# Kernel tuning notes

Measured on AMD Instinct MI355X. Metric: run time of the kernel, lower is better.

## Reference

```python
import jax, jax.numpy as jnp
import numpy as np

EMB = 1024
HEADS = 16
HEAD_DIM = EMB // HEADS

def setup_inputs() -> dict:
    key = jax.random.key(0)
    ks = jax.random.split(key, 12)
    s = 0.02
    x = jax.random.normal(ks[0], (2, 2048, EMB), dtype=jnp.float32)
    return {
        "x": x,
        "wq": jax.random.normal(ks[1], (EMB, EMB), jnp.float32) * s,
        "bq": jnp.zeros((EMB,), jnp.float32),
        "wk": jax.random.normal(ks[2], (EMB, EMB), jnp.float32) * s,
        "bk": jnp.zeros((EMB,), jnp.float32),
        "wv": jax.random.normal(ks[3], (EMB, EMB), jnp.float32) * s,
        "bv": jnp.zeros((EMB,), jnp.float32),
        "wo": jax.random.normal(ks[4], (EMB, EMB), jnp.float32) * s,
        "bo": jnp.zeros((EMB,), jnp.float32),
        "gamma": jnp.ones((EMB,), jnp.float32),
        "beta": jnp.zeros((EMB,), jnp.float32),
    }

def _layernorm(x, gamma, beta, eps=1e-5):
    mu = jnp.mean(x, axis=-1, keepdims=True)
    var = jnp.mean(jnp.square(x - mu), axis=-1, keepdims=True)
    return (x - mu) * jax.lax.rsqrt(var + eps) * gamma + beta

def reference(x, wq, bq, wk, bk, wv, bv, wo, bo, gamma, beta):
    B, T, D = x.shape
    H, d_k = HEADS, HEAD_DIM
    # Linear(y = x W^T + b), then split heads
    q = (x @ wq.T + bq).reshape(B, T, H, d_k)
    k = (x @ wk.T + bk).reshape(B, T, H, d_k)
    v = (x @ wv.T + bv).reshape(B, T, H, d_k)
    scores = jnp.einsum('bthd,bshd->bhts', q, k) / jnp.sqrt(jnp.float32(d_k))
    attn = jax.nn.softmax(scores, axis=-1)  # dropout is identity in eval mode
    out = jnp.einsum('bhts,bshd->bthd', attn, v).reshape(B, T, D)
    out = out @ wo.T + bo
    return _layernorm(x + out, gamma, beta)
```

## Files before the change

kernel.cpp:

```cpp
#include <hip/hip_runtime.h>
#include <stdint.h>
#include <stddef.h>


typedef __bf16 bf16_t;
typedef bf16_t bf16x8 __attribute__((ext_vector_type(8)));
typedef float f32x16 __attribute__((ext_vector_type(16)));
typedef uint16_t u16x8 __attribute__((ext_vector_type(8)));

#define MFMA32(a, b, c) __builtin_amdgcn_mfma_f32_32x32x16_bf16((a), (b), (c), 0, 0, 0)

__device__ __forceinline__ uint16_t f2bf(float f) {
  __bf16 h = (__bf16)f;
  return *(uint16_t*)&h;
}

__device__ __forceinline__ void gload16(const void* g, void* l) {
  __builtin_amdgcn_global_load_lds((const __attribute__((address_space(1))) void*)g,
                                   (__attribute__((address_space(3))) void*)l,
                                   16, 0, 0);
}

__global__ __launch_bounds__(256) void cvt_all(
    const float* __restrict__ x, const float* __restrict__ wq,
    const float* __restrict__ wk, const float* __restrict__ wv,
    const float* __restrict__ wo, uint16_t* __restrict__ xb,
    uint16_t* __restrict__ wqb, uint16_t* __restrict__ wkb,
    uint16_t* __restrict__ wvb, uint16_t* __restrict__ wob) {
  const int gid = blockIdx.x * 256 + threadIdx.x;
  const float* src; uint16_t* dst; int off;
  if (gid < 1048576) {
    src = x; dst = xb; off = gid;
  } else {
    const int t = gid - 1048576;
    off = t & 262143;
    switch (t >> 18) {
      case 0: src = wq; dst = wqb; break;
      case 1: src = wk; dst = wkb; break;
      case 2: src = wv; dst = wvb; break;
      default: src = wo; dst = wob; break;
    }
  }
  const float4 f = ((const float4*)src)[off];
  uint64_t p = (uint64_t)f2bf(f.x) | ((uint64_t)f2bf(f.y) << 16) |
               ((uint64_t)f2bf(f.z) << 32) | ((uint64_t)f2bf(f.w) << 48);
  ((uint64_t*)dst)[off] = p;
}

template <bool OUT_BF16>
__device__ __forceinline__ void gemm128(const uint16_t* __restrict__ A,
                                        const uint16_t* __restrict__ Bt,
                                        const float* __restrict__ bias,
                                        float oscale,
                                        uint16_t* __restrict__ outb,
                                        float* __restrict__ outf) {
  __shared__ uint16_t sA[2][128 * 32];
  __shared__ uint16_t sB[2][128 * 32];
  const int tid = threadIdx.x;
  const int lane = tid & 63, w = tid >> 6;
  const int l31 = lane & 31, half = lane >> 5;
  const int m0 = blockIdx.y * 128, n0 = blockIdx.x * 128;
  const int wm = (w >> 1) * 64, wn = (w & 1) * 64;

  const int ch0 = tid, ch1 = tid + 256;
  const int r0 = ch0 >> 2, g0 = (((ch0 & 3) ^ (r0 & 3)) << 3);
  const int r1 = ch1 >> 2, g1 = (((ch1 & 3) ^ (r1 & 3)) << 3);
  const uint16_t* a0 = A + (size_t)(m0 + r0) * 1024 + g0;
  const uint16_t* a1 = A + (size_t)(m0 + r1) * 1024 + g1;
  const uint16_t* b0 = Bt + (size_t)(n0 + r0) * 1024 + g0;
  const uint16_t* b1 = Bt + (size_t)(n0 + r1) * 1024 + g1;

  gload16(a0, &sA[0][ch0 * 8]);
  gload16(a1, &sA[0][ch1 * 8]);
  gload16(b0, &sB[0][ch0 * 8]);
  gload16(b1, &sB[0][ch1 * 8]);

  f32x16 acc[2][2] = {};

  for (int kt = 0; kt < 32; ++kt) {
    __syncthreads();
    const int cur = kt & 1;
    if (kt < 31) {
      const int ko = (kt + 1) * 32;
      const int nxt = cur ^ 1;
      gload16(a0 + ko, &sA[nxt][ch0 * 8]);
      gload16(a1 + ko, &sA[nxt][ch1 * 8]);
      gload16(b0 + ko, &sB[nxt][ch0 * 8]);
      gload16(b1 + ko, &sB[nxt][ch1 * 8]);
    }
#pragma unroll
    for (int s = 0; s < 2; ++s) {
      const int c = s * 2 + half;
      bf16x8 af[2], bfr[2];
#pragma unroll
      for (int i = 0; i < 2; ++i) {
        const int arow = wm + i * 32 + l31;
        af[i] = *(const bf16x8*)&sA[cur][arow * 32 + ((c ^ (arow & 3)) << 3)];
      }
#pragma unroll
      for (int j = 0; j < 2; ++j) {
        const int brow = wn + j * 32 + l31;
        bfr[j] = *(const bf16x8*)&sB[cur][brow * 32 + ((c ^ (brow & 3)) << 3)];
      }
#pragma unroll
      for (int i = 0; i < 2; ++i)
#pragma unroll
        for (int j = 0; j < 2; ++j) acc[i][j] = MFMA32(af[i], bfr[j], acc[i][j]);
    }
  }

#pragma unroll
  for (int i = 0; i < 2; ++i) {
#pragma unroll
    for (int j = 0; j < 2; ++j) {
      const int gn = n0 + wn + j * 32 + l31;
      const float bv = bias[gn];
#pragma unroll
      for (int reg = 0; reg < 16; ++reg) {
        const int gm = m0 + wm + i * 32 + (reg & 3) + 8 * (reg >> 2) + 4 * half;
        const float v = (acc[i][j][reg] + bv) * oscale;
        const size_t idx = (size_t)gm * 1024 + gn;
        if constexpr (OUT_BF16) outb[idx] = f2bf(v);
        else outf[idx] = v;
      }
    }
  }
}

#define QSCALE 0.18033688011112042f

__global__ __launch_bounds__(256) void qkv_gemm(
    const uint16_t* __restrict__ xb, const uint16_t* __restrict__ wqb,
    const uint16_t* __restrict__ wkb, const uint16_t* __restrict__ wvb,
    const float* __restrict__ bq, const float* __restrict__ bk,
    const float* __restrict__ bv, uint16_t* __restrict__ qb,
    uint16_t* __restrict__ kb, uint16_t* __restrict__ vb) {
  const uint16_t* Bt; const float* bias; uint16_t* out; float sc;
  if (blockIdx.z == 0)      { Bt = wqb; bias = bq; out = qb; sc = QSCALE; }
  else if (blockIdx.z == 1) { Bt = wkb; bias = bk; out = kb; sc = 1.f; }
  else                      { Bt = wvb; bias = bv; out = vb; sc = 1.f; }
  gemm128<true>(xb, Bt, bias, sc, out, nullptr);
}

__global__ __launch_bounds__(256) void o_gemm(const uint16_t* __restrict__ ab,
                                              const uint16_t* __restrict__ wob,
                                              const float* __restrict__ bo,
                                              float* __restrict__ y) {
  gemm128<false>(ab, wob, bo, 1.f, nullptr, y);
}

__global__ __launch_bounds__(256) void v_trans(const uint16_t* __restrict__ vb,
                                               uint16_t* __restrict__ vbT) {
  __shared__ uint16_t sT[64 * 136];
  const int tid = threadIdx.x;
  const int t0 = blockIdx.x * 128;
  const int h = blockIdx.y, b = blockIdx.z;
#pragma unroll
  for (int c = 0; c < 4; ++c) {
    const int idx = c * 256 + tid;
    const int t = idx >> 3, d8 = (idx & 7) * 8;
    u16x8 v = *(const u16x8*)&vb[(size_t)(b * 2048 + t0 + t) * 1024 + h * 64 + d8];
#pragma unroll
    for (int e = 0; e < 8; ++e) sT[(d8 + e) * 136 + t] = v[e];
  }
  __syncthreads();
  const size_t obase = ((size_t)(b * 16 + h) * 64) * 2048 + t0;
#pragma unroll
  for (int c = 0; c < 4; ++c) {
    const int idx = c * 256 + tid;
    const int d = idx >> 4, t8 = (idx & 15) * 8;
    u16x8 v = *(const u16x8*)&sT[d * 136 + t8];
    *(u16x8*)&vbT[obase + (size_t)d * 2048 + t8] = v;
  }
}

__global__ __launch_bounds__(256) void attn(const uint16_t* __restrict__ qb,
                                            const uint16_t* __restrict__ kb,
                                            const uint16_t* __restrict__ vbT,
                                            uint16_t* __restrict__ ab) {
  __shared__ uint16_t sK[2][64 * 64];
  __shared__ uint16_t sV[2][64 * 64];
  __shared__ uint16_t sP[4][32 * 64];
  const int tid = threadIdx.x;
  const int lane = tid & 63, w = tid >> 6;
  const int l31 = lane & 31, half = lane >> 5;
  const int hb = blockIdx.x;
  const int h = hb & 15, b = hb >> 4;
  const int q0 = blockIdx.y * 128;
  const size_t qkbase = (size_t)b * 2048 * 1024 + (size_t)h * 64;
  const size_t vtbase = (size_t)hb * 64 * 2048;

  const int ch0 = tid, ch1 = tid + 256;
  const int r0 = ch0 >> 3, g0 = (((ch0 & 7) ^ (r0 & 7)) << 3);
  const int r1 = ch1 >> 3, g1 = (((ch1 & 7) ^ (r1 & 7)) << 3);
  const uint16_t* k0 = kb + qkbase + (size_t)r0 * 1024 + g0;
  const uint16_t* k1 = kb + qkbase + (size_t)r1 * 1024 + g1;
  const uint16_t* v0 = vbT + vtbase + (size_t)r0 * 2048 + g0;
  const uint16_t* v1 = vbT + vtbase + (size_t)r1 * 2048 + g1;

  gload16(k0, &sK[0][ch0 * 8]);
  gload16(k1, &sK[0][ch1 * 8]);
  gload16(v0, &sV[0][ch0 * 8]);
  gload16(v1, &sV[0][ch1 * 8]);

  bf16x8 qa[4];
  {
    const uint16_t* qrow =
        qb + qkbase + (size_t)(q0 + w * 32 + l31) * 1024 + half * 8;
#pragma unroll
    for (int s = 0; s < 4; ++s) qa[s] = *(const bf16x8*)(qrow + s * 16);
  }

  f32x16 acc_o[2] = {};
  float li[16];
#pragma unroll
  for (int r = 0; r < 16; ++r) li[r] = 0.f;

  uint16_t* sPw = sP[w];
  __bf16* sPb = (__bf16*)sPw;

  for (int kt = 0; kt < 32; ++kt) {
    __syncthreads();
    const int cur = kt & 1;
    if (kt < 31) {
      const size_t so = (size_t)(kt + 1) * 64;
      const int nxt = cur ^ 1;
      gload16(k0 + so * 1024, &sK[nxt][ch0 * 8]);
      gload16(k1 + so * 1024, &sK[nxt][ch1 * 8]);
      gload16(v0 + so, &sV[nxt][ch0 * 8]);
      gload16(v1 + so, &sV[nxt][ch1 * 8]);
    }

    f32x16 acc_s[2] = {};
#pragma unroll
    for (int s = 0; s < 4; ++s) {
      const int c = s * 2 + half;
#pragma unroll
      for (int n = 0; n < 2; ++n) {
        const int brow = n * 32 + l31;
        const bf16x8 kk =
            *(const bf16x8*)&sK[cur][brow * 64 + ((c ^ (brow & 7)) << 3)];
        acc_s[n] = MFMA32(qa[s], kk, acc_s[n]);
      }
    }

#pragma unroll
    for (int reg = 0; reg < 16; ++reg) {
      const int row = (reg & 3) + 8 * (reg >> 2) + 4 * half;
#pragma unroll
      for (int n = 0; n < 2; ++n) {
        const float p = __builtin_amdgcn_exp2f(acc_s[n][reg]);
        li[reg] += p;
        const int col = n * 32 + l31;
        sPb[row * 64 + (((col >> 3) ^ (row & 7)) << 3) + (col & 7)] = (__bf16)p;
      }
    }

#pragma unroll
    for (int s = 0; s < 4; ++s) {
      const int c = s * 2 + half;
      const bf16x8 pa =
          *(const bf16x8*)&sPw[l31 * 64 + ((c ^ (l31 & 7)) << 3)];
#pragma unroll
      for (int n = 0; n < 2; ++n) {
        const int vrow = n * 32 + l31;
        const bf16x8 vv =
            *(const bf16x8*)&sV[cur][vrow * 64 + ((c ^ (vrow & 7)) << 3)];
        acc_o[n] = MFMA32(pa, vv, acc_o[n]);
      }
    }
  }

#pragma unroll
  for (int reg = 0; reg < 16; ++reg) {
    float s = li[reg];
#pragma unroll
    for (int o = 1; o < 32; o <<= 1) s += __shfl_xor(s, o);
    li[reg] = 1.f / s;
  }

#pragma unroll
  for (int n = 0; n < 2; ++n)
#pragma unroll
    for (int reg = 0; reg < 16; ++reg) {
      const int row = q0 + w * 32 + (reg & 3) + 8 * (reg >> 2) + 4 * half;
      const int col = h * 64 + n * 32 + l31;
      ab[(size_t)(b * 2048 + row) * 1024 + col] = f2bf(acc_o[n][reg] * li[reg]);
    }
}

__global__ __launch_bounds__(256) void resid_ln(const float* __restrict__ x,
                                                const float* __restrict__ y,
                                                const float* __restrict__ gamma,
                                                const float* __restrict__ beta,
                                                float* __restrict__ out) {
  const int row = blockIdx.x, tid = threadIdx.x;
  const size_t base = (size_t)row * 1024 + tid * 4;
  const float4 xv = *(const float4*)(x + base);
  const float4 yv = *(const float4*)(y + base);
  const float a = xv.x + yv.x, b2 = xv.y + yv.y, c = xv.z + yv.z, d = xv.w + yv.w;
  float s = a + b2 + c + d;
#pragma unroll
  for (int o = 1; o < 64; o <<= 1) s += __shfl_xor(s, o);
  __shared__ float red[4];
  const int w = tid >> 6;
  if ((tid & 63) == 0) red[w] = s;
  __syncthreads();
  const float mu = (red[0] + red[1] + red[2] + red[3]) * (1.f / 1024.f);
  const float da = a - mu, db = b2 - mu, dc = c - mu, dd = d - mu;
  float sq = da * da + db * db + dc * dc + dd * dd;
#pragma unroll
  for (int o = 1; o < 64; o <<= 1) sq += __shfl_xor(sq, o);
  __syncthreads();
  if ((tid & 63) == 0) red[w] = sq;
  __syncthreads();
  const float var = (red[0] + red[1] + red[2] + red[3]) * (1.f / 1024.f);
  const float rs = rsqrtf(var + 1e-5f);
  const float4 g = *(const float4*)(gamma + tid * 4);
  const float4 bt = *(const float4*)(beta + tid * 4);
  float4 o4;
  o4.x = da * rs * g.x + bt.x;
  o4.y = db * rs * g.y + bt.y;
  o4.z = dc * rs * g.z + bt.z;
  o4.w = dd * rs * g.w + bt.w;
  *(float4*)(out + base) = o4;
}

extern "C" void kernel_launch(void* const* d_in, const int* in_sizes, int n_in,
                              void* d_out, int out_size, void* d_ws, size_t ws_size,
                              hipStream_t stream) {
  const float* x     = (const float*)d_in[0];
  const float* wq    = (const float*)d_in[1];
  const float* bq    = (const float*)d_in[2];
  const float* wk    = (const float*)d_in[3];
  const float* bk    = (const float*)d_in[4];
  const float* wv    = (const float*)d_in[5];
  const float* bv    = (const float*)d_in[6];
  const float* wo    = (const float*)d_in[7];
  const float* bo    = (const float*)d_in[8];
  const float* gamma = (const float*)d_in[9];
  const float* beta  = (const float*)d_in[10];
  float* out = (float*)d_out;
  char* ws = (char*)d_ws;
  const size_t MB = 1024 * 1024;
  uint16_t* xb  = (uint16_t*)(ws);
  uint16_t* ab  = xb;
  uint16_t* wqb = (uint16_t*)(ws + 8 * MB);
  uint16_t* wkb = (uint16_t*)(ws + 10 * MB);
  uint16_t* wvb = (uint16_t*)(ws + 12 * MB);
  uint16_t* wob = (uint16_t*)(ws + 14 * MB);
  uint16_t* qb  = (uint16_t*)(ws + 16 * MB);
  uint16_t* kb  = (uint16_t*)(ws + 24 * MB);
  uint16_t* vb  = (uint16_t*)(ws + 32 * MB);
  uint16_t* vbT = (uint16_t*)(ws + 40 * MB);
  float*    y   = (float*)(ws + 16 * MB);

  cvt_all<<<8192, 256, 0, stream>>>(x, wq, wk, wv, wo, xb, wqb, wkb, wvb, wob);
  qkv_gemm<<<dim3(8, 32, 3), 256, 0, stream>>>(xb, wqb, wkb, wvb, bq, bk, bv, qb, kb, vb);
  v_trans<<<dim3(16, 16, 2), 256, 0, stream>>>(vb, vbT);
  attn<<<dim3(32, 16), 256, 0, stream>>>(qb, kb, vbT, ab);
  o_gemm<<<dim3(8, 32), 256, 0, stream>>>(ab, wob, bo, y);
  resid_ln<<<4096, 256, 0, stream>>>(x, y, gamma, beta, out);
}
```

Baseline: 226.2 us.

## Split attention KV tiles across two wave groups with 512-thread blocks

The attention kernel now runs 8 waves per block. Two groups of four waves each take half of a 128-key tile, so each block loads 128 keys per iteration and runs 16 iterations instead of 32. The P tile is processed in 32-column halves per wave to cut LDS use, and partial outputs and row sums are merged through shared memory at the end. This adds parallel waves per block and halves the barrier count, at the cost of a cross-group reduction and more LDS per block, which may limit occupancy.

```diff
diff --git a/kernel.cpp b/kernel.cpp
--- a/kernel.cpp
+++ b/kernel.cpp
@@ -174,41 +174,45 @@
   }
 }
 
-__global__ __launch_bounds__(256) void attn(const uint16_t* __restrict__ qb,
-                                            const uint16_t* __restrict__ kb,
-                                            const uint16_t* __restrict__ vbT,
-                                            uint16_t* __restrict__ ab) {
-  __shared__ uint16_t sK[2][64 * 64];
-  __shared__ uint16_t sV[2][64 * 64];
-  __shared__ uint16_t sP[4][32 * 64];
+__global__ __launch_bounds__(512, 4) void attn(const uint16_t* __restrict__ qb,
+                                               const uint16_t* __restrict__ kb,
+                                               const uint16_t* __restrict__ vbT,
+                                               uint16_t* __restrict__ ab) {
+  __shared__ __align__(16) uint16_t smem[40960];
+  uint16_t* sK = smem;
+  uint16_t* sV = smem + 16384;
+  uint16_t* sP = smem + 32768;
   const int tid = threadIdx.x;
   const int lane = tid & 63, w = tid >> 6;
   const int l31 = lane & 31, half = lane >> 5;
+  const int rg = w & 3, sh = w >> 2;
   const int hb = blockIdx.x;
   const int h = hb & 15, b = hb >> 4;
   const int q0 = blockIdx.y * 128;
   const size_t qkbase = (size_t)b * 2048 * 1024 + (size_t)h * 64;
   const size_t vtbase = (size_t)hb * 64 * 2048;
 
-  const int ch0 = tid, ch1 = tid + 256;
-  const int r0 = ch0 >> 3, g0 = (((ch0 & 7) ^ (r0 & 7)) << 3);
-  const int r1 = ch1 >> 3, g1 = (((ch1 & 7) ^ (r1 & 7)) << 3);
-  const uint16_t* k0 = kb + qkbase + (size_t)r0 * 1024 + g0;
-  const uint16_t* k1 = kb + qkbase + (size_t)r1 * 1024 + g1;
-  const uint16_t* v0 = vbT + vtbase + (size_t)r0 * 2048 + g0;
-  const uint16_t* v1 = vbT + vtbase + (size_t)r1 * 2048 + g1;
-
-  gload16(k0, &sK[0][ch0 * 8]);
-  gload16(k1, &sK[0][ch1 * 8]);
-  gload16(v0, &sV[0][ch0 * 8]);
-  gload16(v1, &sV[0][ch1 * 8]);
+  const int ch0 = tid, ch1 = tid + 512;
+  const int kr0 = ch0 >> 3, kg0 = (((ch0 & 7) ^ (kr0 & 7)) << 3);
+  const int kr1 = ch1 >> 3, kg1 = (((ch1 & 7) ^ (kr1 & 7)) << 3);
+  const int vr0 = ch0 >> 4, vg0 = (((ch0 & 15) ^ (vr0 & 15)) << 3);
+  const int vr1 = ch1 >> 4, vg1 = (((ch1 & 15) ^ (vr1 & 15)) << 3);
+  const uint16_t* k0 = kb + qkbase + (size_t)kr0 * 1024 + kg0;
+  const uint16_t* k1 = kb + qkbase + (size_t)kr1 * 1024 + kg1;
+  const uint16_t* v0 = vbT + vtbase + (size_t)vr0 * 2048 + vg0;
+  const uint16_t* v1 = vbT + vtbase + (size_t)vr1 * 2048 + vg1;
+
+  gload16(k0, sK + ch0 * 8);
+  gload16(k1, sK + ch1 * 8);
+  gload16(v0, sV + ch0 * 8);
+  gload16(v1, sV + ch1 * 8);
 
   bf16x8 qa[4];
   {
     const uint16_t* qrow =
-        qb + qkbase + (size_t)(q0 + w * 32 + l31) * 1024 + half * 8;
-#pragma unroll
-    for (int s = 0; s < 4; ++s) qa[s] = *(const bf16x8*)(qrow + s * 16);
+        qb + qkbase + (size_t)(q0 + rg * 32 + l31) * 1024 + half * 8;
+#pragma unroll
+    for (int s4 = 0; s4 < 4; ++s4) qa[s4] = *(const bf16x8*)(qrow + s4 * 16);
   }
 
   f32x16 acc_o[2] = {};
@@ -216,77 +220,99 @@
 #pragma unroll
   for (int r = 0; r < 16; ++r) li[r] = 0.f;
 
-  uint16_t* sPw = sP[w];
+  uint16_t* sPw = sP + w * 1024;
   __bf16* sPb = (__bf16*)sPw;
 
-  for (int kt = 0; kt < 32; ++kt) {
+  for (int kt = 0; kt < 16; ++kt) {
     __syncthreads();
     const int cur = kt & 1;
-    if (kt < 31) {
-      const size_t so = (size_t)(kt + 1) * 64;
+    if (kt < 15) {
+      const size_t soK = (size_t)(kt + 1) * 128 * 1024;
+      const int soV = (kt + 1) * 128;
       const int nxt = cur ^ 1;
-      gload16(k0 + so * 1024, &sK[nxt][ch0 * 8]);
-      gload16(k1 + so * 1024, &sK[nxt][ch1 * 8]);
-      gload16(v0 + so, &sV[nxt][ch0 * 8]);
-      gload16(v1 + so, &sV[nxt][ch1 * 8]);
-    }
+      gload16(k0 + soK, sK + nxt * 8192 + ch0 * 8);
+      gload16(k1 + soK, sK + nxt * 8192 + ch1 * 8);
+      gload16(v0 + soV, sV + nxt * 8192 + ch0 * 8);
+      gload16(v1 + soV, sV + nxt * 8192 + ch1 * 8);
+    }
+    const uint16_t* sKc = sK + cur * 8192;
+    const uint16_t* sVc = sV + cur * 8192;
 
     f32x16 acc_s[2] = {};
 #pragma unroll
-    for (int s = 0; s < 4; ++s) {
-      const int c = s * 2 + half;
+    for (int s4 = 0; s4 < 4; ++s4) {
+      const int c = s4 * 2 + half;
 #pragma unroll
       for (int n = 0; n < 2; ++n) {
-        const int brow = n * 32 + l31;
+        const int brow = sh * 64 + n * 32 + l31;
         const bf16x8 kk =
-            *(const bf16x8*)&sK[cur][brow * 64 + ((c ^ (brow & 7)) << 3)];
-        acc_s[n] = MFMA32(qa[s], kk, acc_s[n]);
-      }
-    }
-
-#pragma unroll
-    for (int reg = 0; reg < 16; ++reg) {
-      const int row = (reg & 3) + 8 * (reg >> 2) + 4 * half;
-#pragma unroll
-      for (int n = 0; n < 2; ++n) {
+            *(const bf16x8*)&sKc[brow * 64 + ((c ^ (brow & 7)) << 3)];
+        acc_s[n] = MFMA32(qa[s4], kk, acc_s[n]);
+      }
+    }
+
+#pragma unroll
+    for (int n = 0; n < 2; ++n) {
+#pragma unroll
+      for (int reg = 0; reg < 16; ++reg) {
         const float p = __builtin_amdgcn_exp2f(acc_s[n][reg]);
         li[reg] += p;
-        const int col = n * 32 + l31;
-        sPb[row * 64 + (((col >> 3) ^ (row & 7)) << 3) + (col & 7)] = (__bf16)p;
-      }
-    }
-
-#pragma unroll
-    for (int s = 0; s < 4; ++s) {
-      const int c = s * 2 + half;
-      const bf16x8 pa =
-          *(const bf16x8*)&sPw[l31 * 64 + ((c ^ (l31 & 7)) << 3)];
-#pragma unroll
-      for (int n = 0; n < 2; ++n) {
-        const int vrow = n * 32 + l31;
-        const bf16x8 vv =
-            *(const bf16x8*)&sV[cur][vrow * 64 + ((c ^ (vrow & 7)) << 3)];
-        acc_o[n] = MFMA32(pa, vv, acc_o[n]);
-      }
-    }
-  }
-
-#pragma unroll
-  for (int reg = 0; reg < 16; ++reg) {
-    float s = li[reg];
-#pragma unroll
-    for (int o = 1; o < 32; o <<= 1) s += __shfl_xor(s, o);
-    li[reg] = 1.f / s;
-  }
-
-#pragma unroll
-  for (int n = 0; n < 2; ++n)
+        const int row = (reg & 3) + 8 * (reg >> 2) + 4 * half;
+        sPb[row * 32 + (((l31 >> 3) ^ (row & 3)) << 3) + (l31 & 7)] = (__bf16)p;
+      }
+#pragma unroll
+      for (int st = 0; st < 2; ++st) {
+        const int c2 = st * 2 + half;
+        const bf16x8 pa = *(const bf16x8*)&sPw[l31 * 32 + ((c2 ^ (l31 & 3)) << 3)];
+#pragma unroll
+        for (int n2 = 0; n2 < 2; ++n2) {
+          const int vrow = n2 * 32 + l31;
+          const int c3 = sh * 8 + n * 4 + st * 2 + half;
+          const bf16x8 vv =
+              *(const bf16x8*)&sVc[vrow * 128 + ((c3 ^ (vrow & 15)) << 3)];
+          acc_o[n2] = MFMA32(pa, vv, acc_o[n2]);
+        }
+      }
+    }
+  }
+
+  __syncthreads();
+  float* ep = (float*)smem;
+  float* epl = (float*)(smem + 16384);
+  if (sh == 1) {
+#pragma unroll
+    for (int n2 = 0; n2 < 2; ++n2)
+#pragma unroll
+      for (int reg = 0; reg < 16; ++reg)
+        ep[((rg * 2 + n2) * 16 + reg) * 64 + lane] = acc_o[n2][reg];
+#pragma unroll
+    for (int reg = 0; reg < 16; ++reg)
+      epl[(rg * 16 + reg) * 64 + lane] = li[reg];
+  }
+  __syncthreads();
+  if (sh == 0) {
+#pragma unroll
+    for (int n2 = 0; n2 < 2; ++n2)
+#pragma unroll
+      for (int reg = 0; reg < 16; ++reg)
+        acc_o[n2][reg] += ep[((rg * 2 + n2) * 16 + reg) * 64 + lane];
 #pragma unroll
     for (int reg = 0; reg < 16; ++reg) {
-      const int row = q0 + w * 32 + (reg & 3) + 8 * (reg >> 2) + 4 * half;
-      const int col = h * 64 + n * 32 + l31;
-      ab[(size_t)(b * 2048 + row) * 1024 + col] = f2bf(acc_o[n][reg] * li[reg]);
-    }
+      float s = li[reg] + epl[(rg * 16 + reg) * 64 + lane];
+#pragma unroll
+      for (int o = 1; o < 32; o <<= 1) s += __shfl_xor(s, o);
+      li[reg] = 1.f / s;
+    }
+#pragma unroll
+    for (int n2 = 0; n2 < 2; ++n2)
+#pragma unroll
+      for (int reg = 0; reg < 16; ++reg) {
+        const int row = q0 + rg * 32 + (reg & 3) + 8 * (reg >> 2) + 4 * half;
+        const int col = h * 64 + n2 * 32 + l31;
+        ab[(size_t)(b * 2048 + row) * 1024 + col] =
+            f2bf(acc_o[n2][reg] * li[reg]);
+      }
+  }
 }
 
 __global__ __launch_bounds__(256) void resid_ln(const float* __restrict__ x,
@@ -358,7 +384,7 @@
   cvt_all<<<8192, 256, 0, stream>>>(x, wq, wk, wv, wo, xb, wqb, wkb, wvb, wob);
   qkv_gemm<<<dim3(8, 32, 3), 256, 0, stream>>>(xb, wqb, wkb, wvb, bq, bk, bv, qb, kb, vb);
   v_trans<<<dim3(16, 16, 2), 256, 0, stream>>>(vb, vbT);
-  attn<<<dim3(32, 16), 256, 0, stream>>>(qb, kb, vbT, ab);
+  attn<<<dim3(32, 16), 512, 0, stream>>>(qb, kb, vbT, ab);
   o_gemm<<<dim3(8, 32), 256, 0, stream>>>(ab, wob, bo, y);
   resid_ln<<<4096, 256, 0, stream>>>(x, y, gamma, beta, out);
 }
```

Measured after the change: 227.0 us. Within noise of the previous version (+0.3%).
